# Kernel tuning notes

Measured on AMD Instinct MI355X. Metric: run time of the kernel, lower is better.

Reference implementation:

```python
import jax, jax.numpy as jnp
import numpy as np

HEADS = 12
DIM_HEAD = 64
SCALE = DIM_HEAD ** -0.5


def setup_inputs() -> dict:
    key = jax.random.key(0)
    ks = jax.random.split(key, 7)
    b, n, dim = 16, 1024, 768
    inner = HEADS * DIM_HEAD
    x = jax.random.normal(ks[0], (b, n, dim), dtype=jnp.float32)
    Wq = jax.random.normal(ks[1], (dim, inner), dtype=jnp.float32) * (dim ** -0.5)
    Wkv = jax.random.normal(ks[2], (dim, 2 * inner), dtype=jnp.float32) * (dim ** -0.5)
    mix_pre = jax.random.normal(ks[3], (HEADS, HEADS), dtype=jnp.float32)
    mix_post = jax.random.normal(ks[4], (HEADS, HEADS), dtype=jnp.float32)
    Wo = jax.random.normal(ks[5], (inner, dim), dtype=jnp.float32) * (inner ** -0.5)
    bo = jnp.zeros((dim,), dtype=jnp.float32)
    return {"x": x, "Wq": Wq, "Wkv": Wkv, "mix_pre": mix_pre,
            "mix_post": mix_post, "Wo": Wo, "bo": bo}


def reference(x, Wq, Wkv, mix_pre, mix_post, Wo, bo):
    b, n, dim = x.shape
    h, d = HEADS, DIM_HEAD
    # projections (context is None -> context = x)
    q = (x @ Wq).reshape(b, n, h, d).transpose(0, 2, 1, 3)        # b h n d
    kv = x @ Wkv
    k = kv[..., : h * d].reshape(b, n, h, d).transpose(0, 2, 1, 3)
    v = kv[..., h * d:].reshape(b, n, h, d).transpose(0, 2, 1, 3)
    # scaled QK^T
    attn = jnp.einsum('bhid,bhjd->bhij', q, k) * SCALE             # b h n n
    # talking-heads pre-softmax: mix over head dim
    attn = jnp.einsum('bhij,hg->bgij', attn, mix_pre)
    attn = jax.nn.softmax(attn, axis=-1)
    # talking-heads post-softmax
    attn = jnp.einsum('bhij,hg->bgij', attn, mix_post)
    out = jnp.einsum('bhij,bhjd->bhid', attn, v)                   # b h n d
    out = out.transpose(0, 2, 1, 3).reshape(b, n, h * d)           # b n (h d)
    return out @ Wo + bo
```

## Files before the change

### kernel.cpp

```cpp
#include <hip/hip_runtime.h>


typedef _Float16 f16;
typedef _Float16 f16x2 __attribute__((ext_vector_type(2)));
typedef _Float16 f16x4 __attribute__((ext_vector_type(4)));
typedef _Float16 f16x8 __attribute__((ext_vector_type(8)));
typedef float f32x4 __attribute__((ext_vector_type(4)));
typedef float fv4 __attribute__((ext_vector_type(4)));

#define MFMA32(a, b, c) __builtin_amdgcn_mfma_f32_16x16x32_f16(a, b, c, 0, 0, 0)
#define MFMA16(a, b, c) __builtin_amdgcn_mfma_f32_16x16x16f16(a, b, c, 0, 0, 0)
#define EXP2(x) __builtin_amdgcn_exp2f(x)

__global__ __launch_bounds__(256) void k_cast_x(const float* __restrict__ x,
                                                f16* __restrict__ xb) {
  int idx = (blockIdx.x * 256 + threadIdx.x) * 8;
  fv4 a = *(const fv4*)(x + idx);
  fv4 b = *(const fv4*)(x + idx + 4);
  f16x8 o;
  o[0] = (f16)a[0]; o[1] = (f16)a[1]; o[2] = (f16)a[2]; o[3] = (f16)a[3];
  o[4] = (f16)b[0]; o[5] = (f16)b[1]; o[6] = (f16)b[2]; o[7] = (f16)b[3];
  *(f16x8*)(xb + idx) = o;
}

__global__ __launch_bounds__(256) void k_prep_w(const float* __restrict__ Wq,
                                                const float* __restrict__ Wkv,
                                                const float* __restrict__ Wo,
                                                f16* __restrict__ Wt,
                                                f16* __restrict__ WoT) {
  int idx = blockIdx.x * 256 + threadIdx.x;
  if (idx < 2304 * 768) {
    int n = idx / 768, k = idx % 768;
    float v = (n < 768) ? Wq[k * 768 + n] * 0.125f
                        : Wkv[k * 1536 + (n - 768)];
    Wt[idx] = (f16)v;
  } else {
    int id2 = idx - 2304 * 768;
    int n = id2 / 768, k = id2 % 768;
    WoT[id2] = (f16)Wo[k * 768 + n];
  }
}

__global__ __launch_bounds__(256) void k_gemm_qkv(const f16* __restrict__ A,
                                                  const f16* __restrict__ Bt,
                                                  f16* __restrict__ qb,
                                                  f16* __restrict__ kb,
                                                  f16* __restrict__ vb) {
  __shared__ f16 As[128 * 72];
  __shared__ f16 Bs[128 * 72];
  const int tid = threadIdx.x;
  const int m0 = blockIdx.y << 7;
  const int n0 = blockIdx.x << 7;
  const int lane = tid & 63, w = tid >> 6;
  const int quad = lane >> 4, col = lane & 15;
  const int wm = (w >> 1) << 6, wn = (w & 1) << 6;
  const f32x4 z4 = {0.f, 0.f, 0.f, 0.f};
  f32x4 acc[4][4];
#pragma unroll
  for (int i = 0; i < 4; ++i)
#pragma unroll
    for (int j = 0; j < 4; ++j) acc[i][j] = z4;

  for (int k0 = 0; k0 < 768; k0 += 64) {
#pragma unroll
    for (int s = 0; s < 4; ++s) {
      int u = s * 256 + tid;
      int row = u >> 3, seg = (u & 7) << 3;
      *(f16x8*)&As[row * 72 + seg] = *(const f16x8*)(A + (m0 + row) * 768 + k0 + seg);
      *(f16x8*)&Bs[row * 72 + seg] = *(const f16x8*)(Bt + (n0 + row) * 768 + k0 + seg);
    }
    __syncthreads();
#pragma unroll
    for (int kk = 0; kk < 64; kk += 32) {
      f16x8 af[4], bf[4];
#pragma unroll
      for (int ic = 0; ic < 4; ++ic)
        af[ic] = *(f16x8*)&As[(wm + ic * 16 + col) * 72 + kk + quad * 8];
#pragma unroll
      for (int jc = 0; jc < 4; ++jc)
        bf[jc] = *(f16x8*)&Bs[(wn + jc * 16 + col) * 72 + kk + quad * 8];
#pragma unroll
      for (int ic = 0; ic < 4; ++ic)
#pragma unroll
        for (int jc = 0; jc < 4; ++jc) acc[ic][jc] = MFMA32(af[ic], bf[jc], acc[ic][jc]);
    }
    __syncthreads();
  }
#pragma unroll
  for (int jc = 0; jc < 4; ++jc) {
    int gn = n0 + wn + jc * 16 + col;
#pragma unroll
    for (int ic = 0; ic < 4; ++ic)
#pragma unroll
      for (int r = 0; r < 4; ++r) {
        int gm = m0 + wm + ic * 16 + (quad << 2) + r;
        int b = gm >> 10, i = gm & 1023;
        f16 v = (f16)acc[ic][jc][r];
        if (gn < 768) {
          int h = gn >> 6, dd = gn & 63;
          qb[(((b * 12 + h) << 10) + i) * 64 + dd] = v;
        } else if (gn < 1536) {
          int t = gn - 768; int h = t >> 6, dd = t & 63;
          kb[(((b * 12 + h) << 10) + i) * 64 + dd] = v;
        } else {
          int t = gn - 1536; int h = t >> 6, dd = t & 63;
          vb[(((b * 12 + h) << 10) + i) * 64 + dd] = v;
        }
      }
  }
}

__global__ __launch_bounds__(256) void k_transpose_v(const f16* __restrict__ vb,
                                                     f16* __restrict__ vt) {
  __shared__ f16 t[64 * 72];
  const int bh = blockIdx.x;
  const int n0 = blockIdx.y << 6;
  const int tid = threadIdx.x;
#pragma unroll
  for (int s = 0; s < 2; ++s) {
    int u = s * 256 + tid;
    int r = u >> 3, c = (u & 7) << 3;
    *(f16x8*)&t[r * 72 + c] = *(const f16x8*)(vb + (bh * 1024 + n0 + r) * 64 + c);
  }
  __syncthreads();
#pragma unroll
  for (int s = 0; s < 2; ++s) {
    int u = s * 256 + tid;
    int d = u >> 3, c = (u & 7) << 3;
    f16x8 o;
#pragma unroll
    for (int e = 0; e < 8; ++e) o[e] = t[(c + e) * 72 + d];
    *(f16x8*)(vt + (bh * 64 + d) * 1024 + n0 + c) = o;
  }
}

__global__ __launch_bounds__(256, 3) void k_attn(
    const f16* __restrict__ qb, const f16* __restrict__ kb, const f16* __restrict__ vt,
    const float* __restrict__ mixp, const float* __restrict__ mixq,
    f16* __restrict__ ob) {
  __shared__ f16 SA[10368];
  __shared__ f16 SB[10368];
  __shared__ float msL[1024];
  __shared__ float lsL[1024];

  const int tid = threadIdx.x;
  const int bid = blockIdx.x;
  const int b  = bid >> 6;
  const int i0 = (bid & 63) << 4;
  const int lane = tid & 63;
  const int w = tid >> 6;
  const int quad = lane >> 4, col = lane & 15;
  const int q4 = quad << 2;
  const int w3 = w * 3;
  const int pairH = w3 + (w & 1);
  const int soloH = (w & 1) ? w3 : w3 + 2;
  const f32x4 z4 = {0.f, 0.f, 0.f, 0.f};

  {
    f16x8 z8 = {};
    for (int z = tid; z < 1296; z += 256) ((f16x8*)SA)[z] = z8;
    for (int z = tid; z < 1296; z += 256) ((f16x8*)SB)[z] = z8;
  }

  f16x4 b_pre, b_post;
#pragma unroll
  for (int e = 0; e < 4; ++e) {
    int k = q4 + e;
    bool ok = (k < 12) && (col < 12);
    b_pre[e]  = ok ? (f16)(mixp[k * 12 + col] * 1.44269504f) : (f16)0.f;
    b_post[e] = ok ? (f16)(mixq[k * 12 + col]) : (f16)0.f;
  }

  f16x8 qf[3][2];
#pragma unroll
  for (int h3 = 0; h3 < 3; ++h3)
#pragma unroll
    for (int kc = 0; kc < 2; ++kc)
      qf[h3][kc] = *(const f16x8*)(qb + (((b * 12 + w3 + h3) << 10) + i0 + col) * 64 +
                                   kc * 32 + quad * 8);
  __syncthreads();

  const int granP = (((pairH >> 2) ^ quad) << 2) + (pairH & 3);
  const int granS = (((soloH >> 2) ^ quad) << 2) + (soloH & 3);
  const int mixOff = (quad ^ (col >> 2)) << 2;

  auto computeS = [&](int j0, f16* Sbuf) {
    f32x4 s[3][2];
#pragma unroll
    for (int h3 = 0; h3 < 3; ++h3) {
      const f16* kbase = kb + (((b * 12 + w3 + h3) << 10) + j0) * 64;
#pragma unroll
      for (int jn = 0; jn < 2; ++jn) {
        f32x4 acc = z4;
#pragma unroll
        for (int kc = 0; kc < 2; ++kc) {
          f16x8 kf = *(const f16x8*)(kbase + (jn * 16 + col) * 64 + kc * 32 + quad * 8);
          acc = MFMA32(qf[h3][kc], kf, acc);
        }
        s[h3][jn] = acc;
      }
    }
    if ((w & 1) == 0) {
#pragma unroll
      for (int jn = 0; jn < 2; ++jn) {
        int base2 = (jn * 16 + col) * 324 + q4 * 20;
#pragma unroll
        for (int r = 0; r < 4; ++r) {
          int b2 = base2 + r * 20;
          f16x2 pk; pk[0] = (f16)s[0][jn][r]; pk[1] = (f16)s[1][jn][r];
          *(f16x2*)&Sbuf[b2 + granP] = pk;
          Sbuf[b2 + granS] = (f16)s[2][jn][r];
        }
      }
    } else {
#pragma unroll
      for (int jn = 0; jn < 2; ++jn) {
        int base2 = (jn * 16 + col) * 324 + q4 * 20;
#pragma unroll
        for (int r = 0; r < 4; ++r) {
          int b2 = base2 + r * 20;
          f16x2 pk; pk[0] = (f16)s[1][jn][r]; pk[1] = (f16)s[2][jn][r];
          *(f16x2*)&Sbuf[b2 + granP] = pk;
          Sbuf[b2 + granS] = (f16)s[0][jn][r];
        }
      }
    }
  };

  float m_run[4], l_run[4];
#pragma unroll
  for (int r = 0; r < 4; ++r) { m_run[r] = -1e30f; l_run[r] = 0.f; }

  for (int t = 0; t < 32; ++t) {
    f16* Sbuf = (t & 1) ? SB : SA;
    computeS(t * 32, Sbuf);
    __syncthreads();
    f32x4 d1[8];
#pragma unroll
    for (int u = 0; u < 8; ++u) {
      f16x4 sf = *(f16x4*)&Sbuf[(w * 8 + u) * 324 + col * 20 + mixOff];
      d1[u] = MFMA16(sf, b_pre, z4);
    }
#pragma unroll
    for (int r = 0; r < 4; ++r) {
      float mt = d1[0][r];
#pragma unroll
      for (int u = 1; u < 8; ++u) mt = fmaxf(mt, d1[u][r]);
      float mnew = fmaxf(m_run[r], mt);
      float se = 0.f;
#pragma unroll
      for (int u = 0; u < 8; ++u) se += EXP2(d1[u][r] - mnew);
      l_run[r] = l_run[r] * EXP2(m_run[r] - mnew) + se;
      m_run[r] = mnew;
    }
  }

#pragma unroll
  for (int r = 0; r < 4; ++r) {
    msL[w * 256 + col * 16 + q4 + r] = m_run[r];
    lsL[w * 256 + col * 16 + q4 + r] = l_run[r];
  }
  __syncthreads();
  float mv[4], il[4];
#pragma unroll
  for (int r = 0; r < 4; ++r) {
    int ix = col * 16 + q4 + r;
    float M = msL[ix];
    M = fmaxf(M, msL[256 + ix]);
    M = fmaxf(M, msL[512 + ix]);
    M = fmaxf(M, msL[768 + ix]);
    float L = 0.f;
#pragma unroll
    for (int wp = 0; wp < 4; ++wp)
      L += lsL[wp * 256 + ix] * EXP2(msL[wp * 256 + ix] - M);
    mv[r] = M; il[r] = 1.f / L;
  }

  f32x4 oa[3][4];
#pragma unroll
  for (int g3 = 0; g3 < 3; ++g3)
#pragma unroll
    for (int dc = 0; dc < 4; ++dc) oa[g3][dc] = z4;

  for (int t = 0; t < 32; ++t) {
    const int j0 = t * 32;
    computeS(j0, SA);
    __syncthreads();
#pragma unroll
    for (int u = 0; u < 8; ++u) {
      int v = w * 8 + u;
      f16x4 sf = *(f16x4*)&SA[v * 324 + col * 20 + mixOff];
      f32x4 d1 = MFMA16(sf, b_pre, z4);
      if (col < 12) {
        int pbase = v * 324 + q4 * 20 + (((col >> 2) ^ quad) << 2) + (col & 3);
#pragma unroll
        for (int r = 0; r < 4; ++r)
          SB[pbase + r * 20] = (f16)(EXP2(d1[r] - mv[r]) * il[r]);
      }
    }
    __syncthreads();
#pragma unroll
    for (int u = 0; u < 8; ++u) {
      int v = w * 8 + u;
      f16x4 pf = *(f16x4*)&SB[v * 324 + col * 20 + mixOff];
      f32x4 d2 = MFMA16(pf, b_post, z4);
      if (col < 12) {
#pragma unroll
        for (int r = 0; r < 4; ++r)
          SA[col * 648 + (q4 + r) * 40 + ((w ^ r) << 3) + u] = (f16)d2[r];
      }
    }
    __syncthreads();
#pragma unroll
    for (int g3 = 0; g3 < 3; ++g3) {
      int gp = w3 + g3;
      f16x8 af = *(f16x8*)&SA[gp * 648 + col * 40 + ((quad ^ (col & 3)) << 3)];
#pragma unroll
      for (int dc = 0; dc < 4; ++dc) {
        f16x8 vf = *(const f16x8*)(vt + (((b * 12 + gp) * 64 + dc * 16 + col) << 10) +
                                   j0 + quad * 8);
        oa[g3][dc] = MFMA32(af, vf, oa[g3][dc]);
      }
    }
    __syncthreads();
  }

#pragma unroll
  for (int g3 = 0; g3 < 3; ++g3) {
    int gp = w3 + g3;
#pragma unroll
    for (int dc = 0; dc < 4; ++dc)
#pragma unroll
      for (int r = 0; r < 4; ++r)
        ob[((b << 10) + i0 + q4 + r) * 768 + gp * 64 + dc * 16 + col] =
            (f16)oa[g3][dc][r];
  }
}

__global__ __launch_bounds__(256) void k_gemm_out(const f16* __restrict__ A,
                                                  const f16* __restrict__ Bt,
                                                  const float* __restrict__ bias,
                                                  float* __restrict__ out) {
  __shared__ f16 As[128 * 72];
  __shared__ f16 Bs[128 * 72];
  const int tid = threadIdx.x;
  const int m0 = blockIdx.y << 7;
  const int n0 = blockIdx.x << 7;
  const int lane = tid & 63, w = tid >> 6;
  const int quad = lane >> 4, col = lane & 15;
  const int wm = (w >> 1) << 6, wn = (w & 1) << 6;
  const f32x4 z4 = {0.f, 0.f, 0.f, 0.f};
  f32x4 acc[4][4];
#pragma unroll
  for (int i = 0; i < 4; ++i)
#pragma unroll
    for (int j = 0; j < 4; ++j) acc[i][j] = z4;

  for (int k0 = 0; k0 < 768; k0 += 64) {
#pragma unroll
    for (int s = 0; s < 4; ++s) {
      int u = s * 256 + tid;
      int row = u >> 3, seg = (u & 7) << 3;
      *(f16x8*)&As[row * 72 + seg] = *(const f16x8*)(A + (m0 + row) * 768 + k0 + seg);
      *(f16x8*)&Bs[row * 72 + seg] = *(const f16x8*)(Bt + (n0 + row) * 768 + k0 + seg);
    }
    __syncthreads();
#pragma unroll
    for (int kk = 0; kk < 64; kk += 32) {
      f16x8 af[4], bf[4];
#pragma unroll
      for (int ic = 0; ic < 4; ++ic)
        af[ic] = *(f16x8*)&As[(wm + ic * 16 + col) * 72 + kk + quad * 8];
#pragma unroll
      for (int jc = 0; jc < 4; ++jc)
        bf[jc] = *(f16x8*)&Bs[(wn + jc * 16 + col) * 72 + kk + quad * 8];
#pragma unroll
      for (int ic = 0; ic < 4; ++ic)
#pragma unroll
        for (int jc = 0; jc < 4; ++jc) acc[ic][jc] = MFMA32(af[ic], bf[jc], acc[ic][jc]);
    }
    __syncthreads();
  }
#pragma unroll
  for (int jc = 0; jc < 4; ++jc) {
    int gn = n0 + wn + jc * 16 + col;
    float bv = bias[gn];
#pragma unroll
    for (int ic = 0; ic < 4; ++ic)
#pragma unroll
      for (int r = 0; r < 4; ++r) {
        int gm = m0 + wm + ic * 16 + (quad << 2) + r;
        out[gm * 768 + gn] = acc[ic][jc][r] + bv;
      }
  }
}

extern "C" void kernel_launch(void* const* d_in, const int* in_sizes, int n_in,
                              void* d_out, int out_size, void* d_ws, size_t ws_size,
                              hipStream_t stream) {
  const float* x    = (const float*)d_in[0];
  const float* Wq   = (const float*)d_in[1];
  const float* Wkv  = (const float*)d_in[2];
  const float* mixp = (const float*)d_in[3];
  const float* mixq = (const float*)d_in[4];
  const float* Wo   = (const float*)d_in[5];
  const float* bo   = (const float*)d_in[6];
  float* out = (float*)d_out;

  char* ws = (char*)d_ws;
  f16* xb  = (f16*)(ws);
  f16* Wt  = (f16*)(ws + 25165824);
  f16* WoT = (f16*)(ws + 28704768);
  f16* qb  = (f16*)(ws + 29884416);
  f16* kb  = (f16*)(ws + 55050240);
  f16* vb  = (f16*)(ws + 80216064);
  f16* vt  = xb;
  f16* obuf = vb;

  k_cast_x<<<dim3(6144), dim3(256), 0, stream>>>(x, xb);
  k_prep_w<<<dim3(9216), dim3(256), 0, stream>>>(Wq, Wkv, Wo, Wt, WoT);
  k_gemm_qkv<<<dim3(18, 128), dim3(256), 0, stream>>>(xb, Wt, qb, kb, vb);
  k_transpose_v<<<dim3(192, 16), dim3(256), 0, stream>>>(vb, vt);
  k_attn<<<dim3(1024), dim3(256), 0, stream>>>(qb, kb, vt, mixp, mixq, obuf);
  k_gemm_out<<<dim3(6, 128), dim3(256), 0, stream>>>(obuf, WoT, bo, out);
}
```

Measured before the change: 957.6 us.

## Fuse talking-heads mixes in registers and overlap PV with next QK in attention

The attention kernel now swaps MFMA operand order so the pre-softmax mix output feeds directly into the post-softmax mix MFMA from registers, removing an LDS round trip and a barrier per tile. The second SB buffer is dropped, and the mixed probabilities go to a smaller PmB buffer that also holds the m/l reductions. With less LDS, launch bounds rise to 4 blocks per CU. The PV accumulation for tile t-1 is moved after computeS of tile t so the two overlap. The first pass gives up double buffering and adds an extra barrier per tile, and the higher occupancy target may tighten the register budget.

```diff
diff --git a/kernel.cpp b/kernel.cpp
--- a/kernel.cpp
+++ b/kernel.cpp
@@ -134,14 +134,14 @@
   }
 }
 
-__global__ __launch_bounds__(256, 3) void k_attn(
+__global__ __launch_bounds__(256, 4) void k_attn(
     const f16* __restrict__ qb, const f16* __restrict__ kb, const f16* __restrict__ vt,
     const float* __restrict__ mixp, const float* __restrict__ mixq,
     f16* __restrict__ ob) {
   __shared__ f16 SA[10368];
-  __shared__ f16 SB[10368];
-  __shared__ float msL[1024];
-  __shared__ float lsL[1024];
+  __shared__ f16 PmB[7968];
+  float* msL = (float*)PmB;
+  float* lsL = (float*)(PmB + 2048);
 
   const int tid = threadIdx.x;
   const int bid = blockIdx.x;
@@ -151,7 +151,7 @@
   const int w = tid >> 6;
   const int quad = lane >> 4, col = lane & 15;
   const int q4 = quad << 2;
-  const int w3 = w * 3;
+  const int w3 = w * 3, w8 = w * 8;
   const int pairH = w3 + (w & 1);
   const int soloH = (w & 1) ? w3 : w3 + 2;
   const f32x4 z4 = {0.f, 0.f, 0.f, 0.f};
@@ -159,16 +159,15 @@
   {
     f16x8 z8 = {};
     for (int z = tid; z < 1296; z += 256) ((f16x8*)SA)[z] = z8;
-    for (int z = tid; z < 1296; z += 256) ((f16x8*)SB)[z] = z8;
-  }
-
-  f16x4 b_pre, b_post;
+  }
+
+  f16x4 a_pre, a_post;
 #pragma unroll
   for (int e = 0; e < 4; ++e) {
     int k = q4 + e;
     bool ok = (k < 12) && (col < 12);
-    b_pre[e]  = ok ? (f16)(mixp[k * 12 + col] * 1.44269504f) : (f16)0.f;
-    b_post[e] = ok ? (f16)(mixq[k * 12 + col]) : (f16)0.f;
+    a_pre[e]  = ok ? (f16)(mixp[k * 12 + col] * 1.44269504f) : (f16)0.f;
+    a_post[e] = ok ? (f16)(mixq[k * 12 + col]) : (f16)0.f;
   }
 
   f16x8 qf[3][2];
@@ -178,13 +177,14 @@
     for (int kc = 0; kc < 2; ++kc)
       qf[h3][kc] = *(const f16x8*)(qb + (((b * 12 + w3 + h3) << 10) + i0 + col) * 64 +
                                    kc * 32 + quad * 8);
-  __syncthreads();
 
   const int granP = (((pairH >> 2) ^ quad) << 2) + (pairH & 3);
   const int granS = (((soloH >> 2) ^ quad) << 2) + (soloH & 3);
   const int mixOff = (quad ^ (col >> 2)) << 2;
-
-  auto computeS = [&](int j0, f16* Sbuf) {
+  const int pmWr = col * 40 + (((w ^ (col & 3))) << 3);
+  const int pmRd = col * 40 + (((quad ^ (col & 3))) << 3);
+
+  auto computeS = [&](int j0) {
     f32x4 s[3][2];
 #pragma unroll
     for (int h3 = 0; h3 < 3; ++h3) {
@@ -208,8 +208,8 @@
         for (int r = 0; r < 4; ++r) {
           int b2 = base2 + r * 20;
           f16x2 pk; pk[0] = (f16)s[0][jn][r]; pk[1] = (f16)s[1][jn][r];
-          *(f16x2*)&Sbuf[b2 + granP] = pk;
-          Sbuf[b2 + granS] = (f16)s[2][jn][r];
+          *(f16x2*)&SA[b2 + granP] = pk;
+          SA[b2 + granS] = (f16)s[2][jn][r];
         }
       }
     } else {
@@ -220,8 +220,8 @@
         for (int r = 0; r < 4; ++r) {
           int b2 = base2 + r * 20;
           f16x2 pk; pk[0] = (f16)s[1][jn][r]; pk[1] = (f16)s[2][jn][r];
-          *(f16x2*)&Sbuf[b2 + granP] = pk;
-          Sbuf[b2 + granS] = (f16)s[0][jn][r];
+          *(f16x2*)&SA[b2 + granP] = pk;
+          SA[b2 + granS] = (f16)s[0][jn][r];
         }
       }
     }
@@ -232,14 +232,13 @@
   for (int r = 0; r < 4; ++r) { m_run[r] = -1e30f; l_run[r] = 0.f; }
 
   for (int t = 0; t < 32; ++t) {
-    f16* Sbuf = (t & 1) ? SB : SA;
-    computeS(t * 32, Sbuf);
+    computeS(t * 32);
     __syncthreads();
     f32x4 d1[8];
 #pragma unroll
     for (int u = 0; u < 8; ++u) {
-      f16x4 sf = *(f16x4*)&Sbuf[(w * 8 + u) * 324 + col * 20 + mixOff];
-      d1[u] = MFMA16(sf, b_pre, z4);
+      f16x4 sf = *(f16x4*)&SA[(w8 + u) * 324 + col * 20 + mixOff];
+      d1[u] = MFMA16(a_pre, sf, z4);
     }
 #pragma unroll
     for (int r = 0; r < 4; ++r) {
@@ -253,18 +252,19 @@
       l_run[r] = l_run[r] * EXP2(m_run[r] - mnew) + se;
       m_run[r] = mnew;
     }
+    if (t < 31) __syncthreads();
   }
 
 #pragma unroll
   for (int r = 0; r < 4; ++r) {
-    msL[w * 256 + col * 16 + q4 + r] = m_run[r];
-    lsL[w * 256 + col * 16 + q4 + r] = l_run[r];
+    msL[w * 256 + (q4 + r) * 16 + col] = m_run[r];
+    lsL[w * 256 + (q4 + r) * 16 + col] = l_run[r];
   }
   __syncthreads();
   float mv[4], il[4];
 #pragma unroll
   for (int r = 0; r < 4; ++r) {
-    int ix = col * 16 + q4 + r;
+    int ix = (q4 + r) * 16 + col;
     float M = msL[ix];
     M = fmaxf(M, msL[256 + ix]);
     M = fmaxf(M, msL[512 + ix]);
@@ -275,6 +275,7 @@
       L += lsL[wp * 256 + ix] * EXP2(msL[wp * 256 + ix] - M);
     mv[r] = M; il[r] = 1.f / L;
   }
+  __syncthreads();
 
   f32x4 oa[3][4];
 #pragma unroll
@@ -283,46 +284,52 @@
     for (int dc = 0; dc < 4; ++dc) oa[g3][dc] = z4;
 
   for (int t = 0; t < 32; ++t) {
-    const int j0 = t * 32;
-    computeS(j0, SA);
+    computeS(t * 32);
+    if (t > 0) {
+      const int jp = (t - 1) * 32;
+#pragma unroll
+      for (int g3 = 0; g3 < 3; ++g3) {
+        int gp = w3 + g3;
+        f16x8 af = *(f16x8*)&PmB[gp * 664 + pmRd];
+#pragma unroll
+        for (int dc = 0; dc < 4; ++dc) {
+          f16x8 vf = *(const f16x8*)(vt + (((b * 12 + gp) * 64 + dc * 16 + col) << 10) +
+                                     jp + quad * 8);
+          oa[g3][dc] = MFMA32(af, vf, oa[g3][dc]);
+        }
+      }
+    }
     __syncthreads();
 #pragma unroll
     for (int u = 0; u < 8; ++u) {
-      int v = w * 8 + u;
-      f16x4 sf = *(f16x4*)&SA[v * 324 + col * 20 + mixOff];
-      f32x4 d1 = MFMA16(sf, b_pre, z4);
-      if (col < 12) {
-        int pbase = v * 324 + q4 * 20 + (((col >> 2) ^ quad) << 2) + (col & 3);
+      f16x4 sf = *(f16x4*)&SA[(w8 + u) * 324 + col * 20 + mixOff];
+      f32x4 d1 = MFMA16(a_pre, sf, z4);
+      f16x4 pb;
+#pragma unroll
+      for (int e = 0; e < 4; ++e)
+        pb[e] = (f16)(EXP2(d1[e] - mv[e]) * il[e]);
+      f32x4 d2 = MFMA16(a_post, pb, z4);
+      if (quad < 3) {
 #pragma unroll
         for (int r = 0; r < 4; ++r)
-          SB[pbase + r * 20] = (f16)(EXP2(d1[r] - mv[r]) * il[r]);
-      }
-    }
-    __syncthreads();
-#pragma unroll
-    for (int u = 0; u < 8; ++u) {
-      int v = w * 8 + u;
-      f16x4 pf = *(f16x4*)&SB[v * 324 + col * 20 + mixOff];
-      f32x4 d2 = MFMA16(pf, b_post, z4);
-      if (col < 12) {
-#pragma unroll
-        for (int r = 0; r < 4; ++r)
-          SA[col * 648 + (q4 + r) * 40 + ((w ^ r) << 3) + u] = (f16)d2[r];
-      }
-    }
-    __syncthreads();
+          PmB[(q4 + r) * 664 + pmWr + u] = (f16)d2[r];
+      }
+    }
+    __syncthreads();
+  }
+  {
+    const int jp = 31 * 32;
 #pragma unroll
     for (int g3 = 0; g3 < 3; ++g3) {
       int gp = w3 + g3;
-      f16x8 af = *(f16x8*)&SA[gp * 648 + col * 40 + ((quad ^ (col & 3)) << 3)];
+      f16x8 af = *(f16x8*)&PmB[gp * 664 + pmRd];
 #pragma unroll
       for (int dc = 0; dc < 4; ++dc) {
         f16x8 vf = *(const f16x8*)(vt + (((b * 12 + gp) * 64 + dc * 16 + col) << 10) +
-                                   j0 + quad * 8);
+                                   jp + quad * 8);
         oa[g3][dc] = MFMA32(af, vf, oa[g3][dc]);
       }
     }
-    __syncthreads();
   }
 
 #pragma unroll
```

New measurement: 910.3 us. -4.9%, faster.
